# Optimization experiments

Measured on AMD Instinct MI355X. Metric: run time of the kernel, lower is better.

## Reference

```python
import jax, jax.numpy as jnp
import numpy as np
import math

B, S, D, H, DFF = 4, 1024, 1024, 16, 4096
DK = D // H
EPS = 1e-5


def setup_inputs() -> dict:
    key = jax.random.key(0)
    ks = jax.random.split(key, 16)
    sc = 0.02
    inp = {
        "x": jax.random.normal(ks[0], (B, S, D), jnp.float32),
        "Wq": jax.random.normal(ks[1], (D, D), jnp.float32) * sc,
        "bq": jnp.zeros((D,), jnp.float32),
        "Wk": jax.random.normal(ks[2], (D, D), jnp.float32) * sc,
        "bk": jnp.zeros((D,), jnp.float32),
        "Wv": jax.random.normal(ks[3], (D, D), jnp.float32) * sc,
        "bv": jnp.zeros((D,), jnp.float32),
        "Wo": jax.random.normal(ks[4], (D, D), jnp.float32) * sc,
        "bo": jnp.zeros((D,), jnp.float32),
        "W1": jax.random.normal(ks[5], (D, DFF), jnp.float32) * sc,
        "b1": jnp.zeros((DFF,), jnp.float32),
        "W2": jax.random.normal(ks[6], (DFF, D), jnp.float32) * sc,
        "b2": jnp.zeros((D,), jnp.float32),
        "g1": jnp.ones((D,), jnp.float32),
        "be1": jnp.zeros((D,), jnp.float32),
        "g2": jnp.ones((D,), jnp.float32),
        "be2": jnp.zeros((D,), jnp.float32),
    }
    return inp


def _layernorm(x, g, b):
    mu = jnp.mean(x, axis=-1, keepdims=True)
    var = jnp.mean(jnp.square(x - mu), axis=-1, keepdims=True)
    return (x - mu) * jax.lax.rsqrt(var + EPS) * g + b


def reference(x, Wq, bq, Wk, bk, Wv, bv, Wo, bo, W1, b1, W2, b2, g1, be1, g2, be2):
    # multi-head self-attention (dropout = identity, eval mode)
    q = (x @ Wq + bq).reshape(B, S, H, DK).transpose(0, 2, 1, 3)  # [B,H,S,DK]
    k = (x @ Wk + bk).reshape(B, S, H, DK).transpose(0, 2, 1, 3)
    v = (x @ Wv + bv).reshape(B, S, H, DK).transpose(0, 2, 1, 3)
    scores = jnp.einsum("bhqd,bhkd->bhqk", q, k) / math.sqrt(DK)
    attn_weights = jax.nn.softmax(scores, axis=-1)
    ctx = jnp.einsum("bhqk,bhkd->bhqd", attn_weights, v)
    ctx = ctx.transpose(0, 2, 1, 3).reshape(B, S, D)
    attn_out = ctx @ Wo + bo
    x = _layernorm(x + attn_out, g1, be1)
    ff = jax.nn.relu(x @ W1 + b1) @ W2 + b2
    x = _layernorm(x + ff, g2, be2)
    return x, attn_weights
```

## Files before the change

kernel.cpp:

```cpp
#include <hip/hip_runtime.h>

typedef unsigned short u16;
typedef __attribute__((ext_vector_type(8))) short bf16x8;
typedef __attribute__((ext_vector_type(4))) float f32x4;

__device__ __forceinline__ u16 f2b(float f) {
  unsigned u = __float_as_uint(f);
  u += 0x7fffu + ((u >> 16) & 1u);
  return (u16)(u >> 16);
}
__device__ __forceinline__ float b2f(u16 v) {
  return __uint_as_float((unsigned)v << 16);
}

__device__ __forceinline__ void gload16(const u16* g, u16* l) {
  __builtin_amdgcn_global_load_lds((__attribute__((address_space(1))) void*)(g),
                                   (__attribute__((address_space(3))) void*)(l), 16, 0, 0);
}

__global__ __launch_bounds__(256) void prep_k(const float* __restrict__ x, u16* __restrict__ xb,
                                              const float* __restrict__ Wq, const float* __restrict__ Wk,
                                              const float* __restrict__ Wv, const float* __restrict__ Wo,
                                              const float* __restrict__ W1, const float* __restrict__ W2,
                                              u16* __restrict__ Wqkvt, u16* __restrict__ Wot,
                                              u16* __restrict__ W1t, u16* __restrict__ W2t) {
  int bid = blockIdx.x;
  if (bid < 4096) {
    int i = bid * 256 + threadIdx.x;
    float4 v = *(const float4*)(x + (size_t)i * 4);
    ushort4 o = make_ushort4(f2b(v.x), f2b(v.y), f2b(v.z), f2b(v.w));
    *(ushort4*)(xb + (size_t)i * 4) = o;
    return;
  }
  __shared__ float t[32][33];
  int tx = threadIdx.x & 31, ty = threadIdx.x >> 5;
  const float* src;
  u16* dst;
  int bx, by, ldsrc, lddst;
  int r = bid - 4096;
  if (r < 4096) {
    int which = r >> 10, rr = r & 1023;
    bx = rr & 31; by = rr >> 5; ldsrc = 1024; lddst = 1024;
    src = which == 0 ? Wq : which == 1 ? Wk : which == 2 ? Wv : Wo;
    dst = which < 3 ? Wqkvt + (size_t)which * 1048576 : Wot;
  } else if (r < 8192) {
    int rr = r - 4096;
    bx = rr & 127; by = rr >> 7; src = W1; dst = W1t; ldsrc = 4096; lddst = 1024;
  } else {
    int rr = r - 8192;
    bx = rr & 31; by = rr >> 5; src = W2; dst = W2t; ldsrc = 1024; lddst = 4096;
  }
  int c0 = bx * 32, r0 = by * 32;
#pragma unroll
  for (int i = 0; i < 4; ++i)
    t[ty + i * 8][tx] = src[(size_t)(r0 + ty + i * 8) * ldsrc + c0 + tx];
  __syncthreads();
#pragma unroll
  for (int i = 0; i < 4; ++i)
    dst[(size_t)(c0 + ty + i * 8) * lddst + r0 + tx] = f2b(t[tx][ty + i * 8]);
}

__global__ __launch_bounds__(256) void transpose_v_k(const u16* __restrict__ qkv,
                                                     u16* __restrict__ vt) {
  __shared__ u16 t[32][33];
  int z = blockIdx.z;
  int b = z >> 4, h = z & 15;
  int s0 = blockIdx.x * 32, d0 = blockIdx.y * 32;
  int tx = threadIdx.x, ty = threadIdx.y;
  const u16* src = qkv + (size_t)(b * 1024) * 3072 + 2048 + h * 64;
  u16* dst = vt + (size_t)z * 65536;
#pragma unroll
  for (int i = 0; i < 4; ++i)
    t[ty + i * 8][tx] = src[(size_t)(s0 + ty + i * 8) * 3072 + d0 + tx];
  __syncthreads();
#pragma unroll
  for (int i = 0; i < 4; ++i)
    dst[(size_t)(d0 + i * 8 + ty) * 1024 + s0 + tx] = t[tx][ty + i * 8];
}

template <int BN, int BIAS, int RELU, int SB16, int SF32, int RESID>
__global__ __launch_bounds__(256) void gemm_k(
    const u16* __restrict__ Ab, long aHi, long aLo, int lda,
    const u16* __restrict__ Bt, long bHi, long bLo, int ldb,
    float* __restrict__ Cf, u16* __restrict__ Cb,
    long cHi, long cLo, int ldc,
    const float* __restrict__ bias, const float* __restrict__ biasB,
    const float* __restrict__ biasC, const float* __restrict__ resid,
    int K, int ZD) {
  constexpr int NT = BN / 32;
  constexpr int CB = (BN * 64 * 2) / 1024;
  __shared__ __align__(128) u16 As[128 * 64];
  __shared__ __align__(128) u16 Bs[BN * 64];

  const int tid = threadIdx.x;
  const int lane = tid & 63;
  const int wave = tid >> 6;
  const int waveM = wave >> 1, waveN = wave & 1;
  const int quad = lane >> 4, l16 = lane & 15;

  const int zb = blockIdx.z / ZD, zr = blockIdx.z % ZD;
  const long aOff = zb * aHi + zr * aLo;
  const long bOff = zb * bHi + zr * bLo;
  const long cOff = zb * cHi + zr * cLo;

  const int row0 = blockIdx.y * 128;
  const int col0 = blockIdx.x * BN;

  const int lr = lane >> 3;
  const int lc = (lane & 7) * 8;

  f32x4 acc[4][NT] = {};

  for (int k0 = 0; k0 < K; k0 += 64) {
    const u16* Ag = Ab + aOff + (long)row0 * lda + k0;
    const u16* Bg = Bt + bOff + (long)col0 * ldb + k0;
#pragma unroll
    for (int c = 0; c < 4; ++c) {
      int ch = c * 4 + wave;
      gload16(Ag + (long)(ch * 8 + lr) * lda + lc, &As[ch * 512]);
    }
#pragma unroll
    for (int c = 0; c < CB / 4; ++c) {
      int ch = c * 4 + wave;
      gload16(Bg + (long)(ch * 8 + lr) * ldb + lc, &Bs[ch * 512]);
    }
    __syncthreads();

    bf16x8 af[4][2], bfr[NT][2];
#pragma unroll
    for (int mi = 0; mi < 4; ++mi)
#pragma unroll
      for (int ks = 0; ks < 2; ++ks)
        af[mi][ks] = *(const bf16x8*)&As[(waveM * 64 + mi * 16 + l16) * 64 + ks * 32 + quad * 8];
#pragma unroll
    for (int ni = 0; ni < NT; ++ni)
#pragma unroll
      for (int ks = 0; ks < 2; ++ks)
        bfr[ni][ks] = *(const bf16x8*)&Bs[(waveN * (BN / 2) + ni * 16 + l16) * 64 + ks * 32 + quad * 8];
#pragma unroll
    for (int ks = 0; ks < 2; ++ks)
#pragma unroll
      for (int mi = 0; mi < 4; ++mi)
#pragma unroll
        for (int ni = 0; ni < NT; ++ni)
          acc[mi][ni] = __builtin_amdgcn_mfma_f32_16x16x32_bf16(af[mi][ks], bfr[ni][ks], acc[mi][ni], 0, 0, 0);
    __syncthreads();
  }

#pragma unroll
  for (int ni = 0; ni < NT; ++ni) {
    int col = col0 + waveN * (BN / 2) + ni * 16 + l16;
    float bv = 0.f;
    if (BIAS == 1) bv = bias[col];
    if (BIAS == 3) bv = col < 1024 ? bias[col] : (col < 2048 ? biasB[col - 1024] : biasC[col - 2048]);
#pragma unroll
    for (int mi = 0; mi < 4; ++mi) {
#pragma unroll
      for (int r = 0; r < 4; ++r) {
        int row = row0 + waveM * 64 + mi * 16 + quad * 4 + r;
        float v = acc[mi][ni][r] + bv;
        if (RELU) v = fmaxf(v, 0.f);
        long idx = cOff + (long)row * ldc + col;
        if (RESID) v += resid[idx];
        if (SF32) Cf[idx] = v;
        if (SB16) Cb[idx] = f2b(v);
      }
    }
  }
}

__global__ __launch_bounds__(256) void attn_fused_k(const u16* __restrict__ qkvb,
                                                    const u16* __restrict__ vtb,
                                                    float* __restrict__ attn,
                                                    u16* __restrict__ ctxb) {
  __shared__ __align__(128) u16 Ks[128 * 64];
  __shared__ __align__(128) u16 Vs[64 * 128];
  __shared__ __align__(128) u16 Ps[64 * 136];
  __shared__ float invs[64];

  const int tid = threadIdx.x;
  const int lane = tid & 63;
  const int w = tid >> 6;
  const int quad = lane >> 4, l16 = lane & 15;

  const int z = blockIdx.y;
  const int b = z >> 4, h = z & 15;
  const u16* Kt = qkvb + (long)b * 3145728 + 1024 + h * 64;
  const u16* Vt = vtb + (long)z * 65536;

  const int qabs = blockIdx.x * 64 + w * 16 + l16;
  const long qrow = ((long)b * 1024 + qabs) * 3072 + h * 64;

  bf16x8 qf0 = *(const bf16x8*)&qkvb[qrow + quad * 8];
  bf16x8 qf1 = *(const bf16x8*)&qkvb[qrow + 32 + quad * 8];

  unsigned p[8][8][2];
  float rowsum = 0.f;
  f32x4 cacc[4] = {};

  const int klr = lane >> 3;
  const int klc = 8 * ((lane & 7) ^ (lane >> 3));
  const int vrow_in = lane >> 4;

#pragma unroll
  for (int nc = 0; nc < 8; ++nc) {
#pragma unroll
    for (int c = 0; c < 4; ++c) {
      int ch = c * 4 + w;
      gload16(Kt + (long)(nc * 128 + ch * 8 + klr) * 3072 + klc, &Ks[ch * 512]);
    }
#pragma unroll
    for (int c = 0; c < 4; ++c) {
      int ch = c * 4 + w;
      int vr = ch * 4 + vrow_in;
      int vc = 8 * ((lane & 15) ^ (vr & 7));
      gload16(Vt + (long)vr * 1024 + nc * 128 + vc, &Vs[ch * 512]);
    }
    __syncthreads();

#pragma unroll
    for (int mi = 0; mi < 8; ++mi) {
      int R = mi * 16 + l16;
      bf16x8 kf0 = *(const bf16x8*)&Ks[R * 64 + 8 * (quad ^ (l16 & 7))];
      bf16x8 kf1 = *(const bf16x8*)&Ks[R * 64 + 8 * ((4 + quad) ^ (l16 & 7))];
      f32x4 acc = {};
      acc = __builtin_amdgcn_mfma_f32_16x16x32_bf16(kf0, qf0, acc, 0, 0, 0);
      acc = __builtin_amdgcn_mfma_f32_16x16x32_bf16(kf1, qf1, acc, 0, 0, 0);
      float e0 = __expf(acc[0] * 0.125f);
      float e1 = __expf(acc[1] * 0.125f);
      float e2 = __expf(acc[2] * 0.125f);
      float e3 = __expf(acc[3] * 0.125f);
      rowsum += (e0 + e1) + (e2 + e3);
      unsigned p0 = (unsigned)f2b(e0) | ((unsigned)f2b(e1) << 16);
      unsigned p1 = (unsigned)f2b(e2) | ((unsigned)f2b(e3) << 16);
      p[nc][mi][0] = p0;
      p[nc][mi][1] = p1;
      *(uint2*)&Ps[(w * 16 + l16) * 136 + mi * 16 + quad * 4] = make_uint2(p0, p1);
    }
    __syncthreads();

    {
      int VR = w * 16 + l16;
#pragma unroll
      for (int ks = 0; ks < 4; ++ks) {
        bf16x8 vf = *(const bf16x8*)&Vs[VR * 128 + 8 * ((ks * 4 + quad) ^ (l16 & 7))];
#pragma unroll
        for (int ni = 0; ni < 4; ++ni) {
          bf16x8 pf = *(const bf16x8*)&Ps[(ni * 16 + l16) * 136 + ks * 32 + quad * 8];
          cacc[ni] = __builtin_amdgcn_mfma_f32_16x16x32_bf16(vf, pf, cacc[ni], 0, 0, 0);
        }
      }
    }
    __syncthreads();
  }

  rowsum += __shfl_xor(rowsum, 16);
  rowsum += __shfl_xor(rowsum, 32);
  float inv = 1.f / rowsum;
  if (quad == 0) invs[w * 16 + l16] = inv;
  __syncthreads();

  u16* ctx_lds = Ks;
#pragma unroll
  for (int ni = 0; ni < 4; ++ni) {
    float iv = invs[ni * 16 + l16];
    unsigned c01 = (unsigned)f2b(cacc[ni][0] * iv) | ((unsigned)f2b(cacc[ni][1] * iv) << 16);
    unsigned c23 = (unsigned)f2b(cacc[ni][2] * iv) | ((unsigned)f2b(cacc[ni][3] * iv) << 16);
    *(uint2*)&ctx_lds[(ni * 16 + l16) * 72 + w * 16 + quad * 4] = make_uint2(c01, c23);
  }
  __syncthreads();
#pragma unroll
  for (int i = 0; i < 2; ++i) {
    int q = w * 16 + (lane >> 3) + i * 8;
    int d0 = (lane & 7) * 8;
    bf16x8 cv = *(const bf16x8*)&ctx_lds[q * 72 + d0];
    long tok = (long)b * 1024 + blockIdx.x * 64 + q;
    *(bf16x8*)&ctxb[tok * 1024 + h * 64 + d0] = cv;
  }

  const long arow = ((long)z * 1024 + qabs) * 1024;
#pragma unroll
  for (int nc = 0; nc < 8; ++nc) {
#pragma unroll
    for (int mi = 0; mi < 8; ++mi) {
      float4 v;
      v.x = b2f((u16)(p[nc][mi][0] & 0xffff)) * inv;
      v.y = b2f((u16)(p[nc][mi][0] >> 16)) * inv;
      v.z = b2f((u16)(p[nc][mi][1] & 0xffff)) * inv;
      v.w = b2f((u16)(p[nc][mi][1] >> 16)) * inv;
      *(float4*)&attn[arow + nc * 128 + mi * 16 + quad * 4] = v;
    }
  }
}

template <int WB16, int ADD>
__global__ __launch_bounds__(256) void add_ln_k(const float* __restrict__ xp,
                                                const float* __restrict__ yp,
                                                const float* __restrict__ g,
                                                const float* __restrict__ bta,
                                                float* __restrict__ of,
                                                u16* __restrict__ ob) {
  long row = blockIdx.x;
  int tid = threadIdx.x;
  float4 v = *(const float4*)(xp + row * 1024 + tid * 4);
  if (ADD) {
    const float4 yv = *(const float4*)(yp + row * 1024 + tid * 4);
    v.x += yv.x; v.y += yv.y; v.z += yv.z; v.w += yv.w;
  }
  float s1 = v.x + v.y + v.z + v.w;
  float s2 = v.x * v.x + v.y * v.y + v.z * v.z + v.w * v.w;
#pragma unroll
  for (int d = 32; d > 0; d >>= 1) {
    s1 += __shfl_xor(s1, d);
    s2 += __shfl_xor(s2, d);
  }
  __shared__ float r1[4], r2[4];
  if ((tid & 63) == 0) { r1[tid >> 6] = s1; r2[tid >> 6] = s2; }
  __syncthreads();
  s1 = r1[0] + r1[1] + r1[2] + r1[3];
  s2 = r2[0] + r2[1] + r2[2] + r2[3];
  float mu = s1 * (1.f / 1024.f);
  float var = s2 * (1.f / 1024.f) - mu * mu;
  float rs = rsqrtf(var + 1e-5f);
  float4 gv = *(const float4*)(g + tid * 4);
  float4 bv = *(const float4*)(bta + tid * 4);
  float4 o;
  o.x = (v.x - mu) * rs * gv.x + bv.x;
  o.y = (v.y - mu) * rs * gv.y + bv.y;
  o.z = (v.z - mu) * rs * gv.z + bv.z;
  o.w = (v.w - mu) * rs * gv.w + bv.w;
  *(float4*)(of + row * 1024 + tid * 4) = o;
  if (WB16) {
    ushort4 ov = make_ushort4(f2b(o.x), f2b(o.y), f2b(o.z), f2b(o.w));
    *(ushort4*)(ob + row * 1024 + tid * 4) = ov;
  }
}

extern "C" void kernel_launch(void* const* d_in, const int* in_sizes, int n_in,
                              void* d_out, int out_size, void* d_ws, size_t ws_size,
                              hipStream_t stream) {
  const float* x   = (const float*)d_in[0];
  const float* Wq  = (const float*)d_in[1];
  const float* bq  = (const float*)d_in[2];
  const float* Wk  = (const float*)d_in[3];
  const float* bk  = (const float*)d_in[4];
  const float* Wv  = (const float*)d_in[5];
  const float* bv  = (const float*)d_in[6];
  const float* Wo  = (const float*)d_in[7];
  const float* bo  = (const float*)d_in[8];
  const float* W1  = (const float*)d_in[9];
  const float* b1  = (const float*)d_in[10];
  const float* W2  = (const float*)d_in[11];
  const float* b2  = (const float*)d_in[12];
  const float* g1  = (const float*)d_in[13];
  const float* be1 = (const float*)d_in[14];
  const float* g2  = (const float*)d_in[15];
  const float* be2 = (const float*)d_in[16];

  float* out = (float*)d_out;
  float* attn = out + 4194304LL;

  char* w = (char*)d_ws;
  size_t off = 0;
  auto alloc = [&](size_t bytes) {
    void* p = w + off;
    off = (off + bytes + 255) & ~(size_t)255;
    return p;
  };
  u16* xb        = (u16*)alloc(8388608);
  u16* Wqkvt     = (u16*)alloc(6291456);
  u16* Wot       = (u16*)alloc(2097152);
  u16* W1t       = (u16*)alloc(8388608);
  u16* W2t       = (u16*)alloc(8388608);
  u16* qkvb      = (u16*)alloc(25165824);
  u16* vtb       = (u16*)alloc(8388608);
  u16* ctxb      = (u16*)alloc(8388608);
  float* attn_o  = (float*)alloc(16777216);
  float* x1      = (float*)alloc(16777216);
  u16* x1b       = (u16*)alloc(8388608);
  u16* ff1b      = (u16*)alloc(33554432);
  float* ff2     = (float*)alloc(16777216);
  (void)ws_size; (void)in_sizes; (void)n_in; (void)out_size;

  prep_k<<<16384, 256, 0, stream>>>(x, xb, Wq, Wk, Wv, Wo, W1, W2, Wqkvt, Wot, W1t, W2t);

  gemm_k<128, 3, 0, 1, 0, 0><<<dim3(24, 32, 1), 256, 0, stream>>>(
      xb, 0, 0, 1024, Wqkvt, 0, 0, 1024,
      nullptr, qkvb, 0, 0, 3072, bq, bk, bv, nullptr, 1024, 1);

  transpose_v_k<<<dim3(32, 2, 64), dim3(32, 8), 0, stream>>>(qkvb, vtb);

  attn_fused_k<<<dim3(16, 64), 256, 0, stream>>>(qkvb, vtb, attn, ctxb);

  gemm_k<64, 1, 0, 0, 1, 1><<<dim3(16, 32, 1), 256, 0, stream>>>(
      ctxb, 0, 0, 1024, Wot, 0, 0, 1024,
      attn_o, nullptr, 0, 0, 1024, bo, nullptr, nullptr, x, 1024, 1);

  add_ln_k<1, 0><<<4096, 256, 0, stream>>>(attn_o, nullptr, g1, be1, x1, x1b);

  gemm_k<128, 1, 1, 1, 0, 0><<<dim3(32, 32, 1), 256, 0, stream>>>(
      x1b, 0, 0, 1024, W1t, 0, 0, 1024,
      nullptr, ff1b, 0, 0, 4096, b1, nullptr, nullptr, nullptr, 1024, 1);

  gemm_k<64, 1, 0, 0, 1, 1><<<dim3(16, 32, 1), 256, 0, stream>>>(
      ff1b, 0, 0, 4096, W2t, 0, 0, 4096,
      ff2, nullptr, 0, 0, 1024, b2, nullptr, nullptr, x1, 4096, 1);

  add_ln_k<0, 0><<<4096, 256, 0, stream>>>(ff2, nullptr, g2, be2, out, nullptr);
}
```

Before: 699.9 us.

## Add 256x256 tiled GEMM kernel with 8 waves for QKV and FFN1 projections

Introduces a new GEMM kernel using 256x256 output tiles, 512 threads (8 waves in a 2x4 grid), double-buffered LDS filled through direct global-to-LDS loads, interleaved prefetch with explicit waitcnt and barriers, and setprio around the MFMA bursts. The QKV projection and the first FFN GEMM switch to it from the 128-tile kernel. The goal is more data reuse per tile and better overlap of loads with compute. In exchange the grids are smaller (192 and 256 blocks) and the kernel uses more registers, so occupancy and tail effects on the GPU's CUs could hurt.

```diff
diff --git a/kernel.cpp b/kernel.cpp
--- a/kernel.cpp
+++ b/kernel.cpp
@@ -162,6 +162,114 @@
         if (RELU) v = fmaxf(v, 0.f);
         long idx = cOff + (long)row * ldc + col;
         if (RESID) v += resid[idx];
+        if (SF32) Cf[idx] = v;
+        if (SB16) Cb[idx] = f2b(v);
+      }
+    }
+  }
+}
+
+template <int BIAS, int RELU, int SB16, int SF32>
+__global__ __launch_bounds__(512, 2) void gemm256_k(
+    const u16* __restrict__ Ab, int lda,
+    const u16* __restrict__ Bt, int ldb,
+    float* __restrict__ Cf, u16* __restrict__ Cb, int ldc,
+    const float* __restrict__ bias, const float* __restrict__ biasB,
+    const float* __restrict__ biasC, int K) {
+  __shared__ __align__(128) u16 As[2][16384];
+  __shared__ __align__(128) u16 Bs[2][16384];
+
+  const int tid = threadIdx.x;
+  const int lane = tid & 63;
+  const int w = tid >> 6;
+  const int waveM = w >> 2, waveN = w & 3;
+  const int quad = lane >> 4, l16 = lane & 15;
+
+  const int row0 = blockIdx.y * 256;
+  const int col0 = blockIdx.x * 256;
+
+  const int srow = lane >> 3;
+  const int scol = ((lane & 7) ^ srow) * 8;
+
+  const u16* Ag = Ab + (long)row0 * lda;
+  const u16* Bg = Bt + (long)col0 * ldb;
+
+  f32x4 acc[8][4] = {};
+  const int NT = K >> 6;
+
+#pragma unroll
+  for (int j = 0; j < 4; ++j) {
+    gload16(Ag + (long)(j * 64 + w * 8 + srow) * lda + scol, &As[0][j * 4096 + w * 512]);
+    gload16(Bg + (long)(j * 64 + w * 8 + srow) * ldb + scol, &Bs[0][j * 4096 + w * 512]);
+  }
+
+  for (int kt = 0; kt < NT; ++kt) {
+    const int cur = kt & 1;
+    const int nxt = cur ^ 1;
+    const bool pre = (kt + 1) < NT;
+    const u16* An = Ag + ((long)(kt + 1) << 6);
+    const u16* Bn = Bg + ((long)(kt + 1) << 6);
+
+    bf16x8 bfr[4][2];
+
+#pragma unroll
+    for (int p = 0; p < 4; ++p) {
+      if (pre) {
+        gload16(An + (long)(p * 64 + w * 8 + srow) * lda + scol, &As[nxt][p * 4096 + w * 512]);
+        gload16(Bn + (long)(p * 64 + w * 8 + srow) * ldb + scol, &Bs[nxt][p * 4096 + w * 512]);
+      }
+      if (p == 0) {
+        if (pre) asm volatile("s_waitcnt vmcnt(2)" ::: "memory");
+        else     asm volatile("s_waitcnt vmcnt(0)" ::: "memory");
+        __builtin_amdgcn_sched_barrier(0);
+        __builtin_amdgcn_s_barrier();
+        __builtin_amdgcn_sched_barrier(0);
+#pragma unroll
+        for (int ni = 0; ni < 4; ++ni) {
+          int rb = waveN * 64 + ni * 16 + l16;
+#pragma unroll
+          for (int ks = 0; ks < 2; ++ks)
+            bfr[ni][ks] = *(const bf16x8*)&Bs[cur][rb * 64 + ((ks * 4 + quad) ^ (rb & 7)) * 8];
+        }
+      }
+      bf16x8 af[2][2];
+#pragma unroll
+      for (int ii = 0; ii < 2; ++ii) {
+        int ra = waveM * 128 + (p * 2 + ii) * 16 + l16;
+#pragma unroll
+        for (int ks = 0; ks < 2; ++ks)
+          af[ii][ks] = *(const bf16x8*)&As[cur][ra * 64 + ((ks * 4 + quad) ^ (ra & 7)) * 8];
+      }
+      __builtin_amdgcn_s_setprio(1);
+#pragma unroll
+      for (int ks = 0; ks < 2; ++ks)
+#pragma unroll
+        for (int ii = 0; ii < 2; ++ii)
+#pragma unroll
+          for (int ni = 0; ni < 4; ++ni)
+            acc[p * 2 + ii][ni] = __builtin_amdgcn_mfma_f32_16x16x32_bf16(
+                af[ii][ks], bfr[ni][ks], acc[p * 2 + ii][ni], 0, 0, 0);
+      __builtin_amdgcn_s_setprio(0);
+      __builtin_amdgcn_sched_barrier(0);
+      __builtin_amdgcn_s_barrier();
+      __builtin_amdgcn_sched_barrier(0);
+    }
+  }
+
+#pragma unroll
+  for (int ni = 0; ni < 4; ++ni) {
+    int col = col0 + waveN * 64 + ni * 16 + l16;
+    float bv = 0.f;
+    if (BIAS == 1) bv = bias[col];
+    if (BIAS == 3) bv = col < 1024 ? bias[col] : (col < 2048 ? biasB[col - 1024] : biasC[col - 2048]);
+#pragma unroll
+    for (int mi = 0; mi < 8; ++mi) {
+#pragma unroll
+      for (int r = 0; r < 4; ++r) {
+        int row = row0 + waveM * 128 + mi * 16 + quad * 4 + r;
+        float v = acc[mi][ni][r] + bv;
+        if (RELU) v = fmaxf(v, 0.f);
+        long idx = (long)row * ldc + col;
         if (SF32) Cf[idx] = v;
         if (SB16) Cb[idx] = f2b(v);
       }
@@ -384,9 +492,8 @@
 
   prep_k<<<16384, 256, 0, stream>>>(x, xb, Wq, Wk, Wv, Wo, W1, W2, Wqkvt, Wot, W1t, W2t);
 
-  gemm_k<128, 3, 0, 1, 0, 0><<<dim3(24, 32, 1), 256, 0, stream>>>(
-      xb, 0, 0, 1024, Wqkvt, 0, 0, 1024,
-      nullptr, qkvb, 0, 0, 3072, bq, bk, bv, nullptr, 1024, 1);
+  gemm256_k<3, 0, 1, 0><<<dim3(12, 16), 512, 0, stream>>>(
+      xb, 1024, Wqkvt, 1024, nullptr, qkvb, 3072, bq, bk, bv, 1024);
 
   transpose_v_k<<<dim3(32, 2, 64), dim3(32, 8), 0, stream>>>(qkvb, vtb);
 
@@ -398,9 +505,8 @@
 
   add_ln_k<1, 0><<<4096, 256, 0, stream>>>(attn_o, nullptr, g1, be1, x1, x1b);
 
-  gemm_k<128, 1, 1, 1, 0, 0><<<dim3(32, 32, 1), 256, 0, stream>>>(
-      x1b, 0, 0, 1024, W1t, 0, 0, 1024,
-      nullptr, ff1b, 0, 0, 4096, b1, nullptr, nullptr, nullptr, 1024, 1);
+  gemm256_k<1, 1, 1, 0><<<dim3(16, 16), 512, 0, stream>>>(
+      x1b, 1024, W1t, 1024, nullptr, ff1b, 4096, b1, nullptr, nullptr, 1024);
 
   gemm_k<64, 1, 0, 0, 1, 1><<<dim3(16, 32, 1), 256, 0, stream>>>(
       ff1b, 0, 0, 4096, W2t, 0, 0, 4096,
```

After: 718.0 us. 2.6% more time.
